# Kernel optimization log

Hardware: AMD Instinct MI355X
Metric: run time of the kernel (lower is better)

## Reference

```python
import jax, jax.numpy as jnp
import numpy as np

N, E, F, H, G, C = 50000, 800000, 128, 64, 512, 10
RATIO = 0.5  # forward arg `ratio` baked as constant


def seg_mean(msgs, idx, n):
    s = jax.ops.segment_sum(msgs, idx, num_segments=n)
    cnt = jax.ops.segment_sum(jnp.ones(idx.shape[0], msgs.dtype), idx, num_segments=n)
    return s / jnp.maximum(cnt, 1.0)[:, None]


def sage(x, src, dst, Wl, bl, Wr, ew=None):
    # PyG SAGEConv: lin_l(mean_{j->i} msg_j) + lin_r(x_i); weighted variant scales messages
    m = x[src] if ew is None else x[src] * ew[:, None]
    agg = seg_mean(m, dst, x.shape[0])
    return agg @ Wl + bl + x @ Wr


def topk_mask(scores, seg, num_graphs, ratio):
    # per-graph (segment) top-k edge selection: keep ceil(ratio*edges_in_graph) highest scores
    e = scores.shape[0]
    counts = jax.ops.segment_sum(jnp.ones(e, jnp.float32), seg, num_segments=num_graphs)
    order = jnp.lexsort((-scores, seg))  # sort by segment, then score descending
    seg_sorted = seg[order]
    starts = jnp.concatenate([jnp.zeros(1, jnp.float32), jnp.cumsum(counts)[:-1]])
    rank = jnp.arange(e, dtype=jnp.float32) - starts[seg_sorted]
    k = jnp.ceil(ratio * counts)
    sel = (rank < k[seg_sorted]).astype(scores.dtype)
    return jnp.zeros(e, scores.dtype).at[order].set(sel)


def setup_inputs():
    key = jax.random.key(0)
    ks = jax.random.split(key, 16)
    w = lambda k, shape, fan: (jax.random.normal(k, shape, jnp.float32) / np.sqrt(fan))
    return {
        'x': jax.random.normal(ks[0], (N, F), jnp.float32),
        'edge_index': jax.random.randint(ks[1], (2, E), 0, N, jnp.int32),
        'batch': jnp.sort(jax.random.randint(ks[2], (N,), 0, G, jnp.int32)),
        'W1l': w(ks[3], (F, H), F), 'b1l': jnp.zeros(H, jnp.float32), 'W1r': w(ks[4], (F, H), F),
        'W2l': w(ks[5], (H, H), H), 'b2l': jnp.zeros(H, jnp.float32), 'W2r': w(ks[6], (H, H), H),
        'W3l': w(ks[7], (H, H), H), 'b3l': jnp.zeros(H, jnp.float32), 'W3r': w(ks[8], (H, H), H),
        'Wlin1': w(ks[9], (H, H), H), 'blin1': jnp.zeros(H, jnp.float32),
        'Wlin2': w(ks[10], (H, C), H), 'blin2': jnp.zeros(C, jnp.float32),
    }


def reference(x, edge_index, batch, W1l, b1l, W1r, W2l, b2l, W2r, W3l, b3l, W3r, Wlin1, blin1, Wlin2, blin2):
    src, dst = edge_index[0], edge_index[1]
    h = jax.nn.relu(sage(x, src, dst, W1l, b1l, W1r))
    edge_scores = jnp.sum(h[src] * h[dst], axis=-1)  # [E]
    seg = batch[src]  # graph id per edge (sections)
    sampled = topk_mask(edge_scores, seg, G, RATIO)
    ew = edge_scores * sampled
    h = jax.nn.relu(sage(h, src, dst, W2l, b2l, W2r, ew))
    h = jax.nn.relu(sage(h, src, dst, W3l, b3l, W3r, ew))
    pooled = seg_mean(h, batch, G)  # global_mean_pool
    z = jax.nn.relu(pooled @ Wlin1 + blin1)
    z = z @ Wlin2 + blin2  # dropout inactive in eval
    return jax.nn.log_softmax(z, axis=-1), sampled
```

## Files before the change

### kernel.cpp

```cpp
#include <hip/hip_runtime.h>
#include <hip/hip_bf16.h>
#include <math.h>

static constexpr int N = 50000;
static constexpr int E = 800000;
static constexpr int F = 128;
static constexpr int H = 64;
static constexpr int G = 512;
static constexpr int C = 10;
static constexpr int CAP = 256;
static constexpr int NWIN = 8;
static constexpr int FILL_BT = 512;

static inline int cdiv(long a, int b) { return (int)((a + b - 1) / b); }

__device__ __forceinline__ float uinv_score(unsigned u) {
  return (u & 0x80000000u) ? __uint_as_float(u & 0x7fffffffu) : __uint_as_float(~u);
}

__global__ void k_deg_goff(const int* __restrict__ dst, const int* __restrict__ batch,
                           int* __restrict__ deg, int* __restrict__ goff) {
  for (int i = blockIdx.x * 256 + threadIdx.x; i < N; i += gridDim.x * 256) {
    int b = batch[i];
    if (i == 0) {
      for (int g = 0; g <= b; ++g) goff[g] = 0;
    } else {
      int p = batch[i - 1];
      for (int g = p + 1; g <= b; ++g) goff[g] = i;
    }
    if (i == N - 1) {
      for (int g = b + 1; g <= G; ++g) goff[g] = N;
    }
  }
  const int4* d4 = (const int4*)dst;
  for (int i = blockIdx.x * 256 + threadIdx.x; i < E / 4; i += gridDim.x * 256) {
    int4 v = d4[i];
    atomicAdd(&deg[v.x], 1);
    atomicAdd(&deg[v.y], 1);
    atomicAdd(&deg[v.z], 1);
    atomicAdd(&deg[v.w], 1);
  }
}

__global__ void k_scan_a(const int* __restrict__ cnt, int* __restrict__ off,
                         int* __restrict__ bsum, int n) {
  __shared__ int wsum[16];
  int tid = threadIdx.x, lane = tid & 63, wv = tid >> 6;
  int idx = blockIdx.x * 4096 + tid * 4;
  int v0 = (idx + 0 < n) ? cnt[idx + 0] : 0;
  int v1 = (idx + 1 < n) ? cnt[idx + 1] : 0;
  int v2 = (idx + 2 < n) ? cnt[idx + 2] : 0;
  int v3 = (idx + 3 < n) ? cnt[idx + 3] : 0;
  int local = v0 + v1 + v2 + v3;
  int inc = local;
  for (int d = 1; d < 64; d <<= 1) {
    int t = __shfl_up(inc, d);
    if (lane >= d) inc += t;
  }
  if (lane == 63) wsum[wv] = inc;
  __syncthreads();
  if (tid < 16) {
    int t = wsum[tid];
    for (int d = 1; d < 16; d <<= 1) {
      int u = __shfl_up(t, d);
      if (tid >= d) t += u;
    }
    wsum[tid] = t;
  }
  __syncthreads();
  int woff = (wv > 0) ? wsum[wv - 1] : 0;
  int excl = woff + inc - local;
  if (idx + 0 < n) off[idx + 0] = excl;
  if (idx + 1 < n) off[idx + 1] = excl + v0;
  if (idx + 2 < n) off[idx + 2] = excl + v0 + v1;
  if (idx + 3 < n) off[idx + 3] = excl + v0 + v1 + v2;
  if (tid == 0) bsum[blockIdx.x] = wsum[15];
}

__global__ void k_scan_c(int* __restrict__ off, int* __restrict__ cursor,
                         const int* __restrict__ bsum, int n, int nb) {
  __shared__ int spre[34];
  int tid = threadIdx.x;
  if (tid < 32) {
    int v = (tid < nb) ? bsum[tid] : 0;
    int inc = v;
    for (int d = 1; d < 32; d <<= 1) {
      int t = __shfl_up(inc, d);
      if (tid >= d) inc += t;
    }
    spre[tid] = inc - v;
  }
  __syncthreads();
  int i = blockIdx.x * 256 + tid;
  if (i < n) {
    int v = off[i] + spre[i >> 12];
    off[i] = v;
    cursor[i] = v;
  } else if (i == n) {
    off[n] = spre[nb];
  }
}

__global__ void k_fill_csr(const int* __restrict__ src, const int* __restrict__ dst,
                           const int* __restrict__ batch, int* __restrict__ cursor,
                           int4* __restrict__ csr4, int* __restrict__ einv) {
  int bpw = gridDim.x / NWIN;
  int win = blockIdx.x / bpw;
  int blk = blockIdx.x - win * bpw;
  int e = blk * FILL_BT + threadIdx.x;
  if (e >= E) return;
  int d = dst[e];
  int lo = win * (N / NWIN);
  int hi = lo + (N / NWIN);
  if (d < lo || d >= hi) return;
  int s = src[e];
  int g = batch[s];
  int slot = atomicAdd(&cursor[d], 1);
  csr4[slot] = make_int4(s, e, d, g);
  einv[e] = slot;
}

template <int K>
__global__ void k_gemm2(const float* __restrict__ in, const float* __restrict__ Wl,
                        const float* __restrict__ Wr, const float* __restrict__ b,
                        float* __restrict__ y, float* __restrict__ r) {
  __shared__ float sx[16][K];
  int lane = threadIdx.x, ty = threadIdx.y;
  int tid = ty * 64 + lane;
  int row0 = blockIdx.x * 16;
  const float4* gsrc = (const float4*)(in + (size_t)row0 * K);
  float4* sdst = (float4*)(&sx[0][0]);
#pragma unroll
  for (int i = tid; i < 16 * K / 4; i += 256) sdst[i] = gsrc[i];
  __syncthreads();
  float al[4], ar[4];
  float bias = b[lane];
#pragma unroll
  for (int j = 0; j < 4; ++j) { al[j] = 0.f; ar[j] = bias; }
#pragma unroll 4
  for (int f = 0; f < K; ++f) {
    float wl = Wl[f * H + lane];
    float wr = Wr[f * H + lane];
#pragma unroll
    for (int j = 0; j < 4; ++j) {
      float xv = sx[ty * 4 + j][f];
      al[j] += xv * wl;
      ar[j] += xv * wr;
    }
  }
#pragma unroll
  for (int j = 0; j < 4; ++j) {
    int row = row0 + ty * 4 + j;
    y[(size_t)row * H + lane] = al[j];
    r[(size_t)row * H + lane] = ar[j];
  }
}

template <int K>
__global__ void k_gemm2h(const float* __restrict__ in, const float* __restrict__ Wl,
                         const float* __restrict__ Wr, const float* __restrict__ b,
                         __hip_bfloat16* __restrict__ y, float* __restrict__ r) {
  __shared__ float sx[16][K];
  int lane = threadIdx.x, ty = threadIdx.y;
  int tid = ty * 64 + lane;
  int row0 = blockIdx.x * 16;
  const float4* gsrc = (const float4*)(in + (size_t)row0 * K);
  float4* sdst = (float4*)(&sx[0][0]);
#pragma unroll
  for (int i = tid; i < 16 * K / 4; i += 256) sdst[i] = gsrc[i];
  __syncthreads();
  float al[4], ar[4];
  float bias = b[lane];
#pragma unroll
  for (int j = 0; j < 4; ++j) { al[j] = 0.f; ar[j] = bias; }
#pragma unroll 4
  for (int f = 0; f < K; ++f) {
    float wl = Wl[f * H + lane];
    float wr = Wr[f * H + lane];
#pragma unroll
    for (int j = 0; j < 4; ++j) {
      float xv = sx[ty * 4 + j][f];
      al[j] += xv * wl;
      ar[j] += xv * wr;
    }
  }
#pragma unroll
  for (int j = 0; j < 4; ++j) {
    int row = row0 + ty * 4 + j;
    y[(size_t)row * H + lane] = __float2bfloat16(al[j]);
    r[(size_t)row * H + lane] = ar[j];
  }
}

__global__ void k_agg1(const float* __restrict__ y, const float* __restrict__ r,
                       const int4* __restrict__ csr4, const int* __restrict__ off,
                       float* __restrict__ out) {
  int node = blockIdx.x * 8 + threadIdx.y;
  int lane = threadIdx.x;
  int q = lane >> 3, c = lane & 7;
  int s0 = off[node], s1 = off[node + 1];
  float4 a0 = make_float4(0.f, 0.f, 0.f, 0.f);
  float4 a1 = make_float4(0.f, 0.f, 0.f, 0.f);
  int i = s0 + q;
  for (; i + 8 < s1; i += 16) {
    int se0 = csr4[i].x;
    int se1 = csr4[i + 8].x;
    const float4* p0 = (const float4*)(y + (size_t)se0 * H);
    const float4* p1 = (const float4*)(y + (size_t)se1 * H);
    float4 u0 = p0[c], v0 = p0[c + 8];
    float4 u1 = p1[c], v1 = p1[c + 8];
    a0.x += u0.x + u1.x; a0.y += u0.y + u1.y; a0.z += u0.z + u1.z; a0.w += u0.w + u1.w;
    a1.x += v0.x + v1.x; a1.y += v0.y + v1.y; a1.z += v0.z + v1.z; a1.w += v0.w + v1.w;
  }
  for (; i < s1; i += 8) {
    int se = csr4[i].x;
    const float4* p = (const float4*)(y + (size_t)se * H);
    float4 u = p[c], v = p[c + 8];
    a0.x += u.x; a0.y += u.y; a0.z += u.z; a0.w += u.w;
    a1.x += v.x; a1.y += v.y; a1.z += v.z; a1.w += v.w;
  }
#pragma unroll
  for (int d = 8; d < 64; d <<= 1) {
    a0.x += __shfl_xor(a0.x, d); a0.y += __shfl_xor(a0.y, d);
    a0.z += __shfl_xor(a0.z, d); a0.w += __shfl_xor(a0.w, d);
    a1.x += __shfl_xor(a1.x, d); a1.y += __shfl_xor(a1.y, d);
    a1.z += __shfl_xor(a1.z, d); a1.w += __shfl_xor(a1.w, d);
  }
  if (q == 0) {
    float inv = 1.f / fmaxf((float)(s1 - s0), 1.f);
    const float4* rp = (const float4*)(r + (size_t)node * H);
    float4 r0 = rp[c], r1 = rp[c + 8];
    float4 o0, o1;
    o0.x = fmaxf(a0.x * inv + r0.x, 0.f); o0.y = fmaxf(a0.y * inv + r0.y, 0.f);
    o0.z = fmaxf(a0.z * inv + r0.z, 0.f); o0.w = fmaxf(a0.w * inv + r0.w, 0.f);
    o1.x = fmaxf(a1.x * inv + r1.x, 0.f); o1.y = fmaxf(a1.y * inv + r1.y, 0.f);
    o1.z = fmaxf(a1.z * inv + r1.z, 0.f); o1.w = fmaxf(a1.w * inv + r1.w, 0.f);
    float4* op = (float4*)(out + (size_t)node * H);
    op[c] = o0; op[c + 8] = o1;
  }
}

__global__ void k_compact(const unsigned char* __restrict__ sel,
                          const int4* __restrict__ csr4, const float* __restrict__ ewc,
                          const int* __restrict__ off, int2* __restrict__ csr2,
                          int* __restrict__ cnt2) {
  int node = blockIdx.x * 8 + threadIdx.y;
  int lane = threadIdx.x;
  int s0 = off[node], s1 = off[node + 1];
  unsigned long long lt = ((unsigned long long)1 << lane) - 1;
  int cum = 0;
  for (int i0 = s0; i0 < s1; i0 += 64) {
    int i = i0 + lane;
    bool f = (i < s1) && sel[i];
    unsigned long long m = __ballot(f);
    if (f) {
      int rank = __popcll(m & lt);
      csr2[s0 + cum + rank] = make_int2(csr4[i].x, __float_as_int(ewc[i]));
    }
    cum += __popcll(m);
  }
  if (lane == 0) cnt2[node] = cum;
}

__global__ void k_agg_w(const __hip_bfloat16* __restrict__ y, const float* __restrict__ r,
                        const int2* __restrict__ csr2, const int* __restrict__ cnt2,
                        const int* __restrict__ off, float* __restrict__ out) {
  int node = blockIdx.x * 8 + threadIdx.y;
  int lane = threadIdx.x;
  int q = lane >> 3, c = lane & 7;
  int b0 = off[node], cn = cnt2[node];
  float a[8] = {0.f, 0.f, 0.f, 0.f, 0.f, 0.f, 0.f, 0.f};
  for (int j = q; j < cn; j += 8) {
    int2 sw = csr2[b0 + j];
    float w = __int_as_float(sw.y);
    uint4 pk = ((const uint4*)((const unsigned short*)y + (size_t)sw.x * H))[c];
    a[0] += w * __uint_as_float(pk.x << 16); a[1] += w * __uint_as_float(pk.x & 0xffff0000u);
    a[2] += w * __uint_as_float(pk.y << 16); a[3] += w * __uint_as_float(pk.y & 0xffff0000u);
    a[4] += w * __uint_as_float(pk.z << 16); a[5] += w * __uint_as_float(pk.z & 0xffff0000u);
    a[6] += w * __uint_as_float(pk.w << 16); a[7] += w * __uint_as_float(pk.w & 0xffff0000u);
  }
#pragma unroll
  for (int d = 8; d < 64; d <<= 1) {
#pragma unroll
    for (int j = 0; j < 8; ++j) a[j] += __shfl_xor(a[j], d);
  }
  if (q == 0) {
    int degn = off[node + 1] - off[node];
    float inv = 1.f / fmaxf((float)degn, 1.f);
    const float4* rp = (const float4*)(r + (size_t)node * H);
    float4 r0 = rp[2 * c], r1 = rp[2 * c + 1];
    float4 o0, o1;
    o0.x = fmaxf(a[0] * inv + r0.x, 0.f); o0.y = fmaxf(a[1] * inv + r0.y, 0.f);
    o0.z = fmaxf(a[2] * inv + r0.z, 0.f); o0.w = fmaxf(a[3] * inv + r0.w, 0.f);
    o1.x = fmaxf(a[4] * inv + r1.x, 0.f); o1.y = fmaxf(a[5] * inv + r1.y, 0.f);
    o1.z = fmaxf(a[6] * inv + r1.z, 0.f); o1.w = fmaxf(a[7] * inv + r1.w, 0.f);
    float4* op = (float4*)(out + (size_t)node * H);
    op[2 * c] = o0; op[2 * c + 1] = o1;
  }
}

__global__ void k_score_csr(const float* __restrict__ h1, const int4* __restrict__ csr4,
                            unsigned* __restrict__ scoreu_csr,
                            unsigned short* __restrict__ seg_csr, int* __restrict__ hist) {
  int lane = threadIdx.x;
  int q = lane >> 4, c = lane & 15;
  int s = (blockIdx.x * 8 + threadIdx.y) * 32 + q * 8;
  int4 se[8];
#pragma unroll
  for (int j = 0; j < 8; ++j) se[j] = csr4[s + j];
  float4 xr[8], yr[8];
#pragma unroll
  for (int j = 0; j < 8; ++j) xr[j] = ((const float4*)(h1 + (size_t)se[j].x * H))[c];
#pragma unroll
  for (int j = 0; j < 8; ++j) yr[j] = ((const float4*)(h1 + (size_t)se[j].z * H))[c];
  float p[8];
#pragma unroll
  for (int j = 0; j < 8; ++j)
    p[j] = yr[j].x * xr[j].x + yr[j].y * xr[j].y + yr[j].z * xr[j].z + yr[j].w * xr[j].w;
#pragma unroll
  for (int d = 1; d < 16; d <<= 1) {
#pragma unroll
    for (int j = 0; j < 8; ++j) p[j] += __shfl_xor(p[j], d);
  }
  if (c == 0) {
#pragma unroll
    for (int j = 0; j < 8; ++j) {
      int g = se[j].w;
      unsigned u = __float_as_uint(p[j]);
      u = (u & 0x80000000u) ? ~u : (u | 0x80000000u);
      scoreu_csr[s + j] = u;
      seg_csr[s + j] = (unsigned short)g;
      atomicAdd(&hist[g * 256 + (int)(u >> 24)], 1);
    }
  }
}

__global__ void k_hist(const unsigned* __restrict__ scoreu, const unsigned short* __restrict__ seg,
                       const unsigned* __restrict__ prefix, int* __restrict__ hist, int pass) {
  int e = (blockIdx.x * 256 + threadIdx.x) * 4;
  if (e >= E) return;
  uint4 u4 = *(const uint4*)(scoreu + e);
  ushort4 s4 = *(const ushort4*)(seg + e);
  unsigned uu[4] = {u4.x, u4.y, u4.z, u4.w};
  int gg[4] = {(int)s4.x, (int)s4.y, (int)s4.z, (int)s4.w};
  int predshift = 32 - 8 * pass;
  int bshift = 24 - 8 * pass;
#pragma unroll
  for (int j = 0; j < 4; ++j) {
    unsigned u = uu[j];
    int g = gg[j];
    if ((u >> predshift) == (prefix[g] >> predshift))
      atomicAdd(&hist[g * 256 + (int)((u >> bshift) & 0xFFu)], 1);
  }
}

__global__ void k_scan(int* __restrict__ hist, unsigned* __restrict__ prefix,
                       int* __restrict__ krem, int pass) {
  int g = blockIdx.x;
  int lane = threadIdx.x;
  int4* row = (int4*)(hist + (size_t)g * 256);
  int4 v = row[lane];
  int vj[4] = {v.x, v.y, v.z, v.w};
  int s = v.x + v.y + v.z + v.w;
  int inc = s;
  for (int d = 1; d < 64; d <<= 1) {
    int t = __shfl_up(inc, d);
    if (lane >= d) inc += t;
  }
  int T = __shfl(inc, 63);
  int k = (pass == 0) ? ((T + 1) >> 1) : krem[g];
  int excl = inc - s;
  int pre[4] = {excl, excl + vj[0], excl + vj[0] + vj[1], excl + vj[0] + vj[1] + vj[2]};
  int bsel_l = -1, newk_l = 0;
  if (k > 0) {
    for (int j = 3; j >= 0; --j) {
      int suf = T - pre[j];
      if (suf >= k) { bsel_l = 4 * lane + j; newk_l = k - (suf - vj[j]); break; }
    }
  }
  unsigned long long mask = __ballot(bsel_l >= 0);
  int bsel = 255, newk = 0;
  if (k > 0 && mask) {
    int hi = 63 - __builtin_clzll(mask);
    bsel = __shfl(bsel_l, hi);
    newk = __shfl(newk_l, hi);
  }
  if (lane == 0) {
    unsigned base = (pass == 0) ? 0u : prefix[g];
    prefix[g] = base | ((unsigned)bsel << (24 - 8 * pass));
    krem[g] = newk;
  }
  row[lane] = make_int4(0, 0, 0, 0);
}

__global__ void k_select(const unsigned* __restrict__ scoreu_csr,
                         const unsigned short* __restrict__ seg_csr,
                         const unsigned* __restrict__ thresh,
                         int* __restrict__ eqcnt, int* __restrict__ eqlist,
                         unsigned char* __restrict__ sel_csr, float* __restrict__ ew_csr) {
  int s = (blockIdx.x * 256 + threadIdx.x) * 4;
  if (s >= E) return;
  uint4 u4 = *(const uint4*)(scoreu_csr + s);
  ushort4 g4 = *(const ushort4*)(seg_csr + s);
  unsigned uu[4] = {u4.x, u4.y, u4.z, u4.w};
  int gg[4] = {(int)g4.x, (int)g4.y, (int)g4.z, (int)g4.w};
  float ew[4];
  unsigned char sl[4];
#pragma unroll
  for (int j = 0; j < 4; ++j) {
    unsigned u = uu[j];
    int g = gg[j];
    unsigned t = thresh[g];
    unsigned um = u & 0xffffff00u;
    float sel = 0.f;
    if (um > t) sel = 1.f;
    else if (um == t) {
      int slot = atomicAdd(&eqcnt[g], 1);
      if (slot < CAP) eqlist[g * CAP + slot] = s + j;
    }
    sl[j] = (unsigned char)sel;
    ew[j] = uinv_score(u) * sel;
  }
  *(uchar4*)(sel_csr + s) = make_uchar4(sl[0], sl[1], sl[2], sl[3]);
  *(float4*)(ew_csr + s) = make_float4(ew[0], ew[1], ew[2], ew[3]);
}

__global__ void k_resolve(const int* __restrict__ krem, const int* __restrict__ eqcnt,
                          const int* __restrict__ eqlist, const int4* __restrict__ csr4,
                          const unsigned* __restrict__ scoreu_csr,
                          unsigned char* __restrict__ sel_csr, float* __restrict__ ew_csr) {
  int g = blockIdx.x * 256 + threadIdx.x;
  if (g >= G) return;
  int c = eqcnt[g]; if (c > CAP) c = CAP;
  int r = krem[g];  if (r > c) r = c;
  const int* lst = eqlist + g * CAP;
  unsigned last_u = 0u; int last_e = -1; bool first = true;
  for (int i = 0; i < r; ++i) {
    unsigned bu = 0u; int be = -1, bs = -1;
    for (int j = 0; j < c; ++j) {
      int slot = lst[j];
      unsigned u = scoreu_csr[slot];
      int eid = csr4[slot].y;
      bool after = first || (u < last_u) || (u == last_u && eid > last_e);
      if (after && (bs < 0 || u > bu || (u == bu && eid < be))) { bu = u; be = eid; bs = slot; }
    }
    if (bs < 0) break;
    sel_csr[bs] = 1;
    ew_csr[bs] = uinv_score(bu);
    last_u = bu; last_e = be; first = false;
  }
}

__global__ void k_sampled(const int* __restrict__ einv, const unsigned char* __restrict__ sel_csr,
                          float* __restrict__ sampled) {
  int e = (blockIdx.x * 256 + threadIdx.x) * 4;
  if (e >= E) return;
  int4 iv = *(const int4*)(einv + e);
  float4 o;
  o.x = (float)sel_csr[iv.x];
  o.y = (float)sel_csr[iv.y];
  o.z = (float)sel_csr[iv.z];
  o.w = (float)sel_csr[iv.w];
  *(float4*)(sampled + e) = o;
}

__global__ void k_poolhead(const float* __restrict__ h3, const int* __restrict__ goff,
                           const float* __restrict__ W1, const float* __restrict__ b1,
                           const float* __restrict__ W2, const float* __restrict__ b2,
                           float* __restrict__ outp) {
  int g = blockIdx.x;
  int tid = threadIdx.x;
  int h = tid & 63, j = tid >> 6;
  int s0 = goff[g], s1 = goff[g + 1];
  float a = 0.f;
  for (int n = s0 + j; n < s1; n += 8) a += h3[(size_t)n * H + h];
  __shared__ float sp[8][H];
  __shared__ float p[H], z1[H], z2[C];
  __shared__ float lse;
  sp[j][h] = a;
  __syncthreads();
  if (j == 0) {
    float s = sp[0][h] + sp[1][h] + sp[2][h] + sp[3][h]
            + sp[4][h] + sp[5][h] + sp[6][h] + sp[7][h];
    float inv = 1.f / fmaxf((float)(s1 - s0), 1.f);
    p[h] = s * inv;
  }
  __syncthreads();
  if (j == 0) {
    float acc = b1[h];
#pragma unroll 8
    for (int f = 0; f < H; ++f) acc += p[f] * W1[f * H + h];
    z1[h] = fmaxf(acc, 0.f);
  }
  __syncthreads();
  if (tid < C) {
    float a2 = b2[tid];
#pragma unroll 8
    for (int f = 0; f < H; ++f) a2 += z1[f] * W2[f * C + tid];
    z2[tid] = a2;
  }
  __syncthreads();
  if (tid == 0) {
    float m = z2[0];
    for (int c = 1; c < C; ++c) m = fmaxf(m, z2[c]);
    float s = 0.f;
    for (int c = 0; c < C; ++c) s += expf(z2[c] - m);
    lse = m + logf(s);
  }
  __syncthreads();
  if (tid < C) outp[(size_t)g * C + tid] = z2[tid] - lse;
}

extern "C" void kernel_launch(void* const* d_in, const int* in_sizes, int n_in,
                              void* d_out, int out_size, void* d_ws, size_t ws_size,
                              hipStream_t stream) {
  const float* x     = (const float*)d_in[0];
  const int*   ei    = (const int*)d_in[1];
  const int*   batch = (const int*)d_in[2];
  const float* W1l   = (const float*)d_in[3];
  const float* b1l   = (const float*)d_in[4];
  const float* W1r   = (const float*)d_in[5];
  const float* W2l   = (const float*)d_in[6];
  const float* b2l   = (const float*)d_in[7];
  const float* W2r   = (const float*)d_in[8];
  const float* W3l   = (const float*)d_in[9];
  const float* b3l   = (const float*)d_in[10];
  const float* W3r   = (const float*)d_in[11];
  const float* Wlin1 = (const float*)d_in[12];
  const float* blin1 = (const float*)d_in[13];
  const float* Wlin2 = (const float*)d_in[14];
  const float* blin2 = (const float*)d_in[15];

  const int* srcv = ei;
  const int* dstv = ei + E;

  float* out_ls   = (float*)d_out;
  float* out_samp = out_ls + G * C;

  char* w = (char*)d_ws;
  auto carve = [&](size_t bytes) { void* p = (void*)w; w += (bytes + 255) & ~(size_t)255; return p; };
  char* zbase   = w;
  int*      deg     = (int*)carve((size_t)N * 4);
  int*      eqcnt   = (int*)carve((size_t)G * 4);
  int*      hist    = (int*)carve((size_t)G * 256 * 4);
  size_t    zbytes  = (size_t)(w - zbase);
  float*    h1      = (float*)carve((size_t)N * H * 4);
  float*    h2      = (float*)carve((size_t)N * H * 4);
  float*    h3      = (float*)carve((size_t)N * H * 4);
  float*    yb      = (float*)carve((size_t)N * H * 4);
  float*    rb      = (float*)carve((size_t)N * H * 4);
  __hip_bfloat16* ybh = (__hip_bfloat16*)carve((size_t)N * H * 2);
  unsigned* scoreu_csr = (unsigned*)carve((size_t)E * 4);
  unsigned short* seg_csr = (unsigned short*)carve((size_t)E * 2);
  float*    ew_csr     = (float*)carve((size_t)E * 4);
  unsigned char* sel_csr = (unsigned char*)carve((size_t)E);
  int4*     csr4    = (int4*)carve((size_t)E * 16);
  int*      einv    = (int*)carve((size_t)E * 4);
  int*      off     = (int*)carve((size_t)(N + 1) * 4);
  int*      cursor  = (int*)carve((size_t)N * 4);
  int*      cnt2    = (int*)carve((size_t)N * 4);
  int*      goff    = (int*)carve((size_t)(G + 1) * 4);
  unsigned* prefix  = (unsigned*)carve((size_t)G * 4);
  int*      krem    = (int*)carve((size_t)G * 4);
  int*      eqlist  = (int*)carve((size_t)G * CAP * 4);
  int*      bsum    = (int*)carve((size_t)16 * 4);
  int2*     csr2    = (int2*)carve((size_t)E * 8);

  hipMemsetAsync(zbase, 0, zbytes, stream);

  k_deg_goff<<<256, 256, 0, stream>>>(dstv, batch, deg, goff);
  int nb = cdiv(N, 4096);
  k_scan_a<<<nb, 1024, 0, stream>>>(deg, off, bsum, N);
  k_scan_c<<<cdiv(N + 1, 256), 256, 0, stream>>>(off, cursor, bsum, N, nb);
  k_fill_csr<<<NWIN * cdiv(E, FILL_BT), FILL_BT, 0, stream>>>(srcv, dstv, batch, cursor,
                                                              csr4, einv);

  k_gemm2<F><<<N / 16, dim3(64, 4), 0, stream>>>(x, W1l, W1r, b1l, yb, rb);
  k_agg1<<<N / 8, dim3(64, 8), 0, stream>>>(yb, rb, csr4, off, h1);

  k_score_csr<<<E / 256, dim3(64, 8), 0, stream>>>(h1, csr4, scoreu_csr, seg_csr, hist);
  k_scan<<<G, 64, 0, stream>>>(hist, prefix, krem, 0);
  for (int p = 1; p <= 2; ++p) {
    k_hist<<<cdiv(E / 4, 256), 256, 0, stream>>>(scoreu_csr, seg_csr, prefix, hist, p);
    k_scan<<<G, 64, 0, stream>>>(hist, prefix, krem, p);
  }
  k_select<<<cdiv(E / 4, 256), 256, 0, stream>>>(scoreu_csr, seg_csr, prefix,
                                                 eqcnt, eqlist, sel_csr, ew_csr);
  k_resolve<<<cdiv(G, 256), 256, 0, stream>>>(krem, eqcnt, eqlist, csr4, scoreu_csr,
                                              sel_csr, ew_csr);
  k_sampled<<<cdiv(E / 4, 256), 256, 0, stream>>>(einv, sel_csr, out_samp);

  k_compact<<<N / 8, dim3(64, 8), 0, stream>>>(sel_csr, csr4, ew_csr, off, csr2, cnt2);

  k_gemm2h<H><<<N / 16, dim3(64, 4), 0, stream>>>(h1, W2l, W2r, b2l, ybh, rb);
  k_agg_w<<<N / 8, dim3(64, 8), 0, stream>>>(ybh, rb, csr2, cnt2, off, h2);

  k_gemm2h<H><<<N / 16, dim3(64, 4), 0, stream>>>(h2, W3l, W3r, b3l, ybh, rb);
  k_agg_w<<<N / 8, dim3(64, 8), 0, stream>>>(ybh, rb, csr2, cnt2, off, h3);

  k_poolhead<<<G, 512, 0, stream>>>(h3, goff, Wlin1, blin1, Wlin2, blin2, out_ls);
}
```

Before: 458.8 us.

## Merge independent kernels into shared launches via block-role partitioning

Three pairs of independent kernels are merged into single launches, with blockIdx used to assign roles: CSR fill with the layer-1 GEMM, edge scoring with the layer-2 GEMM, and the sampled-mask scatter with CSR compaction. This cuts launch count and lets independent work share the GPU concurrently, filling idle CUs during small or latency-bound phases. The costs are divergent block roles within one grid and possible uneven scheduling, and the layer-2 GEMM now shares its grid with the scoring blocks.

Result: faster. 424.6 us (-7.5%).

```diff
diff --git a/kernel.cpp b/kernel.cpp
--- a/kernel.cpp
+++ b/kernel.cpp
@@ -10,7 +10,10 @@
 static constexpr int C = 10;
 static constexpr int CAP = 256;
 static constexpr int NWIN = 8;
-static constexpr int FILL_BT = 512;
+static constexpr int EB = E / 256;
+static constexpr int GB1 = N / 16;
+static constexpr int GB2 = (N + 31) / 32;
+static constexpr int SB = E / 256;
 
 static inline int cdiv(long a, int b) { return (int)((a + b - 1) / b); }
 
@@ -101,58 +104,58 @@
   }
 }
 
-__global__ void k_fill_csr(const int* __restrict__ src, const int* __restrict__ dst,
-                           const int* __restrict__ batch, int* __restrict__ cursor,
-                           int4* __restrict__ csr4, int* __restrict__ einv) {
-  int bpw = gridDim.x / NWIN;
-  int win = blockIdx.x / bpw;
-  int blk = blockIdx.x - win * bpw;
-  int e = blk * FILL_BT + threadIdx.x;
-  if (e >= E) return;
-  int d = dst[e];
-  int lo = win * (N / NWIN);
-  int hi = lo + (N / NWIN);
-  if (d < lo || d >= hi) return;
-  int s = src[e];
-  int g = batch[s];
-  int slot = atomicAdd(&cursor[d], 1);
-  csr4[slot] = make_int4(s, e, d, g);
-  einv[e] = slot;
-}
-
-template <int K>
-__global__ void k_gemm2(const float* __restrict__ in, const float* __restrict__ Wl,
-                        const float* __restrict__ Wr, const float* __restrict__ b,
-                        float* __restrict__ y, float* __restrict__ r) {
-  __shared__ float sx[16][K];
+__global__ void k_fill_gemm(const int* __restrict__ src, const int* __restrict__ dst,
+                            const int* __restrict__ batch, int* __restrict__ cursor,
+                            int4* __restrict__ csr4, int* __restrict__ einv,
+                            const float* __restrict__ x, const float* __restrict__ Wl,
+                            const float* __restrict__ Wr, const float* __restrict__ bl,
+                            float* __restrict__ y, float* __restrict__ r) {
+  __shared__ float sx[16][F];
   int lane = threadIdx.x, ty = threadIdx.y;
-  int tid = ty * 64 + lane;
-  int row0 = blockIdx.x * 16;
-  const float4* gsrc = (const float4*)(in + (size_t)row0 * K);
-  float4* sdst = (float4*)(&sx[0][0]);
-#pragma unroll
-  for (int i = tid; i < 16 * K / 4; i += 256) sdst[i] = gsrc[i];
-  __syncthreads();
-  float al[4], ar[4];
-  float bias = b[lane];
-#pragma unroll
-  for (int j = 0; j < 4; ++j) { al[j] = 0.f; ar[j] = bias; }
+  int bq = blockIdx.x / 9, br = blockIdx.x - bq * 9;
+  if (br == 0) {
+    int tid = ty * 64 + lane;
+    int row0 = bq * 16;
+    const float4* gsrc = (const float4*)(x + (size_t)row0 * F);
+    float4* sdst = (float4*)(&sx[0][0]);
+#pragma unroll
+    for (int i = tid; i < 16 * F / 4; i += 256) sdst[i] = gsrc[i];
+    __syncthreads();
+    float al[4], ar[4];
+    float bias = bl[lane];
+#pragma unroll
+    for (int j = 0; j < 4; ++j) { al[j] = 0.f; ar[j] = bias; }
 #pragma unroll 4
-  for (int f = 0; f < K; ++f) {
-    float wl = Wl[f * H + lane];
-    float wr = Wr[f * H + lane];
+    for (int f = 0; f < F; ++f) {
+      float wl = Wl[f * H + lane];
+      float wr = Wr[f * H + lane];
+#pragma unroll
+      for (int j = 0; j < 4; ++j) {
+        float xv = sx[ty * 4 + j][f];
+        al[j] += xv * wl;
+        ar[j] += xv * wr;
+      }
+    }
 #pragma unroll
     for (int j = 0; j < 4; ++j) {
-      float xv = sx[ty * 4 + j][f];
-      al[j] += xv * wl;
-      ar[j] += xv * wr;
-    }
-  }
-#pragma unroll
-  for (int j = 0; j < 4; ++j) {
-    int row = row0 + ty * 4 + j;
-    y[(size_t)row * H + lane] = al[j];
-    r[(size_t)row * H + lane] = ar[j];
+      int row = row0 + ty * 4 + j;
+      y[(size_t)row * H + lane] = al[j];
+      r[(size_t)row * H + lane] = ar[j];
+    }
+  } else {
+    int tid = ty * 64 + lane;
+    int fid = bq * 8 + (br - 1);
+    int win = fid / EB;
+    int blk = fid - win * EB;
+    int e = blk * 256 + tid;
+    int d = dst[e];
+    int lo = win * (N / NWIN), hi = lo + (N / NWIN);
+    if (d < lo || d >= hi) return;
+    int s = src[e];
+    int g = batch[s];
+    int slot = atomicAdd(&cursor[d], 1);
+    csr4[slot] = make_int4(s, e, d, g);
+    einv[e] = slot;
   }
 }
 
@@ -240,28 +243,6 @@
   }
 }
 
-__global__ void k_compact(const unsigned char* __restrict__ sel,
-                          const int4* __restrict__ csr4, const float* __restrict__ ewc,
-                          const int* __restrict__ off, int2* __restrict__ csr2,
-                          int* __restrict__ cnt2) {
-  int node = blockIdx.x * 8 + threadIdx.y;
-  int lane = threadIdx.x;
-  int s0 = off[node], s1 = off[node + 1];
-  unsigned long long lt = ((unsigned long long)1 << lane) - 1;
-  int cum = 0;
-  for (int i0 = s0; i0 < s1; i0 += 64) {
-    int i = i0 + lane;
-    bool f = (i < s1) && sel[i];
-    unsigned long long m = __ballot(f);
-    if (f) {
-      int rank = __popcll(m & lt);
-      csr2[s0 + cum + rank] = make_int2(csr4[i].x, __float_as_int(ewc[i]));
-    }
-    cum += __popcll(m);
-  }
-  if (lane == 0) cnt2[node] = cum;
-}
-
 __global__ void k_agg_w(const __hip_bfloat16* __restrict__ y, const float* __restrict__ r,
                         const int2* __restrict__ csr2, const int* __restrict__ cnt2,
                         const int* __restrict__ off, float* __restrict__ out) {
@@ -299,38 +280,78 @@
   }
 }
 
-__global__ void k_score_csr(const float* __restrict__ h1, const int4* __restrict__ csr4,
+__global__ void k_score_g2h(const float* __restrict__ h1, const int4* __restrict__ csr4,
                             unsigned* __restrict__ scoreu_csr,
-                            unsigned short* __restrict__ seg_csr, int* __restrict__ hist) {
-  int lane = threadIdx.x;
-  int q = lane >> 4, c = lane & 15;
-  int s = (blockIdx.x * 8 + threadIdx.y) * 32 + q * 8;
-  int4 se[8];
-#pragma unroll
-  for (int j = 0; j < 8; ++j) se[j] = csr4[s + j];
-  float4 xr[8], yr[8];
-#pragma unroll
-  for (int j = 0; j < 8; ++j) xr[j] = ((const float4*)(h1 + (size_t)se[j].x * H))[c];
-#pragma unroll
-  for (int j = 0; j < 8; ++j) yr[j] = ((const float4*)(h1 + (size_t)se[j].z * H))[c];
-  float p[8];
-#pragma unroll
-  for (int j = 0; j < 8; ++j)
-    p[j] = yr[j].x * xr[j].x + yr[j].y * xr[j].y + yr[j].z * xr[j].z + yr[j].w * xr[j].w;
-#pragma unroll
-  for (int d = 1; d < 16; d <<= 1) {
-#pragma unroll
-    for (int j = 0; j < 8; ++j) p[j] += __shfl_xor(p[j], d);
-  }
-  if (c == 0) {
-#pragma unroll
-    for (int j = 0; j < 8; ++j) {
-      int g = se[j].w;
-      unsigned u = __float_as_uint(p[j]);
-      u = (u & 0x80000000u) ? ~u : (u | 0x80000000u);
-      scoreu_csr[s + j] = u;
-      seg_csr[s + j] = (unsigned short)g;
-      atomicAdd(&hist[g * 256 + (int)(u >> 24)], 1);
+                            unsigned short* __restrict__ seg_csr, int* __restrict__ hist,
+                            const float* __restrict__ Wl, const float* __restrict__ Wr,
+                            const float* __restrict__ bl,
+                            __hip_bfloat16* __restrict__ y, float* __restrict__ r) {
+  __shared__ float sx[32][H];
+  int lane = threadIdx.x, ty = threadIdx.y;
+  int q3 = blockIdx.x / 3, r3 = blockIdx.x - q3 * 3;
+  if (r3 == 0 && q3 < GB2) {
+    int tid = ty * 64 + lane;
+    int row0 = q3 * 32;
+    {
+      int row = row0 + (tid >> 4);
+      if (row < N)
+        ((float4*)(&sx[0][0]))[tid] = ((const float4*)h1)[(size_t)row * (H / 4) + (tid & 15)];
+    }
+    __syncthreads();
+    float al[4], ar[4];
+    float bias = bl[lane];
+#pragma unroll
+    for (int j = 0; j < 4; ++j) { al[j] = 0.f; ar[j] = bias; }
+#pragma unroll 4
+    for (int f = 0; f < H; ++f) {
+      float wl = Wl[f * H + lane];
+      float wr = Wr[f * H + lane];
+#pragma unroll
+      for (int j = 0; j < 4; ++j) {
+        float xv = sx[ty * 4 + j][f];
+        al[j] += xv * wl;
+        ar[j] += xv * wr;
+      }
+    }
+#pragma unroll
+    for (int j = 0; j < 4; ++j) {
+      int row = row0 + ty * 4 + j;
+      if (row < N) {
+        y[(size_t)row * H + lane] = __float2bfloat16(al[j]);
+        r[(size_t)row * H + lane] = ar[j];
+      }
+    }
+  } else {
+    int sid = blockIdx.x - (q3 + (r3 > 0 ? 1 : 0));
+    int q = lane >> 4, c = lane & 15;
+    int s = (sid * 8 + ty) * 32 + q * 8;
+    int4 se[8];
+#pragma unroll
+    for (int j = 0; j < 8; ++j) se[j] = csr4[s + j];
+    float4 xr[8], yr[8];
+#pragma unroll
+    for (int j = 0; j < 8; ++j) xr[j] = ((const float4*)(h1 + (size_t)se[j].x * H))[c];
+#pragma unroll
+    for (int j = 0; j < 8; ++j) yr[j] = ((const float4*)(h1 + (size_t)se[j].z * H))[c];
+    float p[8];
+#pragma unroll
+    for (int j = 0; j < 8; ++j)
+      p[j] = yr[j].x * xr[j].x + yr[j].y * xr[j].y + yr[j].z * xr[j].z + yr[j].w * xr[j].w;
+#pragma unroll
+    for (int d = 1; d < 16; d <<= 1) {
+#pragma unroll
+      for (int j = 0; j < 8; ++j) p[j] += __shfl_xor(p[j], d);
+    }
+    if (c == 0) {
+#pragma unroll
+      for (int j = 0; j < 8; ++j) {
+        int g = se[j].w;
+        unsigned u = __float_as_uint(p[j]);
+        u = (u & 0x80000000u) ? ~u : (u | 0x80000000u);
+        scoreu_csr[s + j] = u;
+        seg_csr[s + j] = (unsigned short)g;
+        atomicAdd(&hist[g * 256 + (int)(u >> 24)], 1);
+      }
     }
   }
 }
@@ -451,17 +472,40 @@
   }
 }
 
-__global__ void k_sampled(const int* __restrict__ einv, const unsigned char* __restrict__ sel_csr,
-                          float* __restrict__ sampled) {
-  int e = (blockIdx.x * 256 + threadIdx.x) * 4;
-  if (e >= E) return;
-  int4 iv = *(const int4*)(einv + e);
-  float4 o;
-  o.x = (float)sel_csr[iv.x];
-  o.y = (float)sel_csr[iv.y];
-  o.z = (float)sel_csr[iv.z];
-  o.w = (float)sel_csr[iv.w];
-  *(float4*)(sampled + e) = o;
+__global__ void k_samp_comp(const unsigned char* __restrict__ sel,
+                            const int4* __restrict__ csr4, const float* __restrict__ ewc,
+                            const int* __restrict__ off, int2* __restrict__ csr2,
+                            int* __restrict__ cnt2,
+                            const int* __restrict__ einv, float* __restrict__ sampled) {
+  int lane = threadIdx.x, ty = threadIdx.y;
+  if (blockIdx.x < N / 8) {
+    int node = blockIdx.x * 8 + ty;
+    int s0 = off[node], s1 = off[node + 1];
+    unsigned long long lt = ((unsigned long long)1 << lane) - 1;
+    int cum = 0;
+    for (int i0 = s0; i0 < s1; i0 += 64) {
+      int i = i0 + lane;
+      bool f = (i < s1) && sel[i];
+      unsigned long long m = __ballot(f);
+      if (f) {
+        int rank = __popcll(m & lt);
+        csr2[s0 + cum + rank] = make_int2(csr4[i].x, __float_as_int(ewc[i]));
+      }
+      cum += __popcll(m);
+    }
+    if (lane == 0) cnt2[node] = cum;
+  } else {
+    int tid = ty * 64 + lane;
+    int e = ((blockIdx.x - N / 8) * 512 + tid) * 4;
+    if (e >= E) return;
+    int4 iv = *(const int4*)(einv + e);
+    float4 o;
+    o.x = (float)sel[iv.x];
+    o.y = (float)sel[iv.y];
+    o.z = (float)sel[iv.z];
+    o.w = (float)sel[iv.w];
+    *(float4*)(sampled + e) = o;
+  }
 }
 
 __global__ void k_poolhead(const float* __restrict__ h3, const int* __restrict__ goff,
@@ -572,13 +616,14 @@
   int nb = cdiv(N, 4096);
   k_scan_a<<<nb, 1024, 0, stream>>>(deg, off, bsum, N);
   k_scan_c<<<cdiv(N + 1, 256), 256, 0, stream>>>(off, cursor, bsum, N, nb);
-  k_fill_csr<<<NWIN * cdiv(E, FILL_BT), FILL_BT, 0, stream>>>(srcv, dstv, batch, cursor,
-                                                              csr4, einv);
-
-  k_gemm2<F><<<N / 16, dim3(64, 4), 0, stream>>>(x, W1l, W1r, b1l, yb, rb);
+
+  k_fill_gemm<<<9 * EB, dim3(64, 4), 0, stream>>>(srcv, dstv, batch, cursor, csr4, einv,
+                                                  x, W1l, W1r, b1l, yb, rb);
+
   k_agg1<<<N / 8, dim3(64, 8), 0, stream>>>(yb, rb, csr4, off, h1);
 
-  k_score_csr<<<E / 256, dim3(64, 8), 0, stream>>>(h1, csr4, scoreu_csr, seg_csr, hist);
+  k_score_g2h<<<SB + GB2, dim3(64, 8), 0, stream>>>(h1, csr4, scoreu_csr, seg_csr, hist,
+                                                    W2l, W2r, b2l, ybh, rb);
   k_scan<<<G, 64, 0, stream>>>(hist, prefix, krem, 0);
   for (int p = 1; p <= 2; ++p) {
     k_hist<<<cdiv(E / 4, 256), 256, 0, stream>>>(scoreu_csr, seg_csr, prefix, hist, p);
@@ -588,11 +633,10 @@
                                                  eqcnt, eqlist, sel_csr, ew_csr);
   k_resolve<<<cdiv(G, 256), 256, 0, stream>>>(krem, eqcnt, eqlist, csr4, scoreu_csr,
                                               sel_csr, ew_csr);
-  k_sampled<<<cdiv(E / 4, 256), 256, 0, stream>>>(einv, sel_csr, out_samp);
-
-  k_compact<<<N / 8, dim3(64, 8), 0, stream>>>(sel_csr, csr4, ew_csr, off, csr2, cnt2);
-
-  k_gemm2h<H><<<N / 16, dim3(64, 4), 0, stream>>>(h1, W2l, W2r, b2l, ybh, rb);
+
+  k_samp_comp<<<N / 8 + cdiv(E / 4, 512), dim3(64, 8), 0, stream>>>(
+      sel_csr, csr4, ew_csr, off, csr2, cnt2, einv, out_samp);
+
   k_agg_w<<<N / 8, dim3(64, 8), 0, stream>>>(ybh, rb, csr2, cnt2, off, h2);
 
   k_gemm2h<H><<<N / 16, dim3(64, 4), 0, stream>>>(h2, W3l, W3r, b3l, ybh, rb);
```
